# Optimization experiments

Hardware: AMD Instinct MI355X
Metric: run time of the kernel (lower is better)

Reference implementation:

```python
import jax, jax.numpy as jnp
import numpy as np

D_MODEL = 1024
N_HEAD = 16
D_H = D_MODEL // N_HEAD


def setup_inputs() -> dict:
    key = jax.random.key(0)
    ks = jax.random.split(key, 5)
    scale = 1.0 / np.sqrt(D_MODEL)
    x = jax.random.normal(ks[0], (4, 2048, D_MODEL), dtype=jnp.float32)
    # torch nn.Linear weights: shape (out_features, in_features)
    W_qkv = jax.random.uniform(ks[1], (3 * D_MODEL, D_MODEL), dtype=jnp.float32, minval=-scale, maxval=scale)
    b_qkv = jax.random.uniform(ks[2], (3 * D_MODEL,), dtype=jnp.float32, minval=-scale, maxval=scale)
    W_o = jax.random.uniform(ks[3], (D_MODEL, D_MODEL), dtype=jnp.float32, minval=-scale, maxval=scale)
    b_o = jax.random.uniform(ks[4], (D_MODEL,), dtype=jnp.float32, minval=-scale, maxval=scale)
    return {"x": x, "W_qkv": W_qkv, "b_qkv": b_qkv, "W_o": W_o, "b_o": b_o}


def reference(x, W_qkv, b_qkv, W_o, b_o):
    B, S, D = x.shape
    qkv = jnp.einsum('bsd,ed->bse', x, W_qkv) + b_qkv  # [B,S,3D]
    q, k, v = jnp.split(qkv, 3, axis=-1)
    # [B,H,S,d_h]
    q = q.reshape(B, S, N_HEAD, D_H).transpose(0, 2, 1, 3)
    k = k.reshape(B, S, N_HEAD, D_H).transpose(0, 2, 1, 3)
    v = v.reshape(B, S, N_HEAD, D_H).transpose(0, 2, 1, 3)
    sim = jnp.einsum('bhqd,bhkd->bhqk', q, k) / jnp.sqrt(jnp.float32(D_H))
    neg_inf = jnp.finfo(sim.dtype).min
    causal = jnp.tril(jnp.ones((S, S), dtype=bool))
    sim = jnp.where(causal[None, None], sim, neg_inf)
    attn = jax.nn.softmax(sim, axis=-1)
    out = jnp.einsum('bhqk,bhkd->bhqd', attn, v)  # [B,H,S,d_h]
    out = out.transpose(0, 2, 1, 3).reshape(B, S, D)
    return jnp.einsum('bsd,ed->bse', out, W_o) + b_o
```

## Files before the change

kernel.cpp:

```cpp
#include <hip/hip_runtime.h>

#define D_MODEL 1024
#define S_LEN   2048
#define BATCH   4
#define NH      16
#define DH      64
#define M_ROWS  (BATCH * S_LEN)

typedef __attribute__((ext_vector_type(8))) short short8;
typedef __attribute__((ext_vector_type(4))) float floatx4;
typedef unsigned short ushort_t;
typedef __attribute__((ext_vector_type(4))) ushort_t ushortx4;

__device__ __forceinline__ ushort_t f2bf(float f) {
    union { float f; unsigned u; } v; v.f = f;
    unsigned r = v.u + 0x7FFFu + ((v.u >> 16) & 1u);
    return (ushort_t)(r >> 16);
}

__device__ __forceinline__ int pack2(float lo, float hi) {
    return (int)__builtin_amdgcn_perm(__float_as_uint(hi), __float_as_uint(lo), 0x07060302u);
}

__device__ __forceinline__ void async_copy16(const ushort_t* g, ushort_t* l) {
    __builtin_amdgcn_global_load_lds(
        (const __attribute__((address_space(1))) void*)g,
        (__attribute__((address_space(3))) void*)l,
        16, 0, 0);
}

#define N0 (M_ROWS * D_MODEL)
#define N1 (3 * D_MODEL * D_MODEL)
#define N2 (D_MODEL * D_MODEL)
#define NQUADS ((N0 + N1 + N2) / 4)

__global__ __launch_bounds__(256)
void cvt_f32_bf16(const float* __restrict__ s0, const float* __restrict__ s1,
                  const float* __restrict__ s2, ushort_t* __restrict__ d0,
                  ushort_t* __restrict__ d1, ushort_t* __restrict__ d2)
{
    const int q = blockIdx.x * 256 + threadIdx.x;
    if (q >= NQUADS) return;
    const float* s; ushort_t* d; int e;
    if (q < N0 / 4)            { s = s0; d = d0; e = q * 4; }
    else if (q < (N0 + N1) / 4){ s = s1; d = d1; e = q * 4 - N0; }
    else                       { s = s2; d = d2; e = q * 4 - N0 - N1; }
    const float4 v = *(const float4*)&s[e];
    ushortx4 o;
    o[0] = f2bf(v.x); o[1] = f2bf(v.y); o[2] = f2bf(v.z); o[3] = f2bf(v.w);
    *(ushortx4*)&d[e] = o;
}

template<bool F32OUT, bool VSPLIT>
__global__ __launch_bounds__(256)
void gemm_bt_bias(const ushort_t* __restrict__ A, const ushort_t* __restrict__ B,
                  const float* __restrict__ bias, void* __restrict__ Cv,
                  ushort_t* __restrict__ vt, int M, int N, int K)
{
    constexpr int BK = 64;
    constexpr float C2 = 0.18033688011112042f;
    __shared__ ushort_t As[128][BK];
    __shared__ ushort_t Bs[128][BK];

    const int tid  = threadIdx.x;
    const int lane = tid & 63;
    const int wave = tid >> 6;
    const int quad = lane >> 4;
    const int l16  = lane & 15;
    const int bm   = blockIdx.y * 128;
    const int bn   = blockIdx.x * 128;
    const int wm   = (wave & 1) * 64;
    const int wn   = (wave >> 1) * 64;

    floatx4 acc[4][4] = {};

    const int l8r = lane >> 3;
    const int c8  = lane & 7;
    const int swz = l16 & 7;

    for (int k0 = 0; k0 < K; k0 += BK) {
        __syncthreads();
        #pragma unroll
        for (int i = wave; i < 16; i += 4) {
            const int row = i * 8 + l8r;
            const int cc  = (c8 ^ l8r) * 8;
            async_copy16(&A[(size_t)(bm + row) * K + k0 + cc], &As[i * 8][0]);
            async_copy16(&B[(size_t)(bn + row) * K + k0 + cc], &Bs[i * 8][0]);
        }
        __syncthreads();

        #pragma unroll
        for (int h = 0; h < 2; h++) {
            short8 af[4], bfr[4];
            #pragma unroll
            for (int i = 0; i < 4; i++)
                af[i]  = *(const short8*)&As[wm + i * 16 + l16][((h * 4 + quad) ^ swz) * 8];
            #pragma unroll
            for (int i = 0; i < 4; i++)
                bfr[i] = *(const short8*)&Bs[wn + i * 16 + l16][((h * 4 + quad) ^ swz) * 8];

            #pragma unroll
            for (int mi = 0; mi < 4; mi++)
                #pragma unroll
                for (int ni = 0; ni < 4; ni++)
                    acc[mi][ni] = __builtin_amdgcn_mfma_f32_16x16x32_bf16(af[mi], bfr[ni], acc[mi][ni], 0, 0, 0);
        }
    }

    #pragma unroll
    for (int ni = 0; ni < 4; ni++) {
        const int col = bn + wn + ni * 16 + l16;
        const float bv = bias[col];
        #pragma unroll
        for (int mi = 0; mi < 4; mi++)
            #pragma unroll
            for (int r = 0; r < 4; r++) {
                const int row = bm + wm + mi * 16 + quad * 4 + r;
                const float val = acc[mi][ni][r] + bv;
                if (VSPLIT) {
                    if (col < 2 * D_MODEL) {
                        const float vv = (col < D_MODEL) ? val * C2 : val;
                        ((ushort_t*)Cv)[(size_t)row * 2048 + col] = f2bf(vv);
                    } else {
                        const int vcol = col - 2 * D_MODEL;
                        const int h = vcol >> 6, dh = vcol & 63;
                        const int b = row >> 11, s = row & 2047;
                        const int sp = (s & ~63) | ((s & 15) << 2) | ((s >> 4) & 3);
                        vt[(((size_t)(b * NH + h)) * DH + dh) * S_LEN + sp] = f2bf(val);
                    }
                } else if (F32OUT) {
                    ((float*)Cv)[(size_t)row * N + col] = val;
                } else {
                    ((ushort_t*)Cv)[(size_t)row * N + col] = f2bf(val);
                }
            }
    }
}

#define BKV 64

struct TileState {
    short8  qf[2];
    floatx4 o[4];
    float   l[4];
};

__device__ __forceinline__ void attn_tile(
    const ushort_t (*__restrict__ Ks)[DH], const ushort_t (*__restrict__ Vs)[BKV],
    ushort_t* __restrict__ Psw, TileState& st, bool diag,
    int wave, int quad, int l16, int swz, short8 ones)
{
    floatx4 sc[4];
    #pragma unroll
    for (int ns = 0; ns < 4; ns++) {
        const short8 kf0 = *(const short8*)&Ks[ns * 16 + l16][(quad ^ swz) * 8];
        const short8 kf1 = *(const short8*)&Ks[ns * 16 + l16][((4 + quad) ^ swz) * 8];
        floatx4 z = {};
        z = __builtin_amdgcn_mfma_f32_16x16x32_bf16(st.qf[0], kf0, z, 0, 0, 0);
        z = __builtin_amdgcn_mfma_f32_16x16x32_bf16(st.qf[1], kf1, z, 0, 0, 0);
        sc[ns] = z;
    }

    #pragma unroll
    for (int r = 0; r < 4; r++) {
        const int qloc = wave * 16 + quad * 4 + r;
        float p[4];
        #pragma unroll
        for (int ns = 0; ns < 4; ns++) {
            float v = sc[ns][r];
            if (diag) {
                const int kj = ns * 16 + l16;
                v = (kj <= qloc) ? v : -1e30f;
            }
            p[ns] = __builtin_amdgcn_exp2f(v);
        }
        int2 w;
        w.x = pack2(p[0], p[1]);
        w.y = pack2(p[2], p[3]);
        const int row = quad * 4 + r;
        *(int2*)((char*)Psw + row * 128 + (((l16 >> 1) ^ (row & 7)) << 4) + ((l16 & 1) << 3)) = w;
    }

    short8 pf[2];
    #pragma unroll
    for (int c = 0; c < 2; c++)
        pf[c] = *(const short8*)((const char*)Psw + l16 * 128 + ((((c << 2) | quad) ^ (l16 & 7)) << 4));

    floatx4 racc = {};
    racc = __builtin_amdgcn_mfma_f32_16x16x32_bf16(pf[0], ones, racc, 0, 0, 0);
    racc = __builtin_amdgcn_mfma_f32_16x16x32_bf16(pf[1], ones, racc, 0, 0, 0);

    #pragma unroll
    for (int r = 0; r < 4; r++)
        st.l[r] += racc[r];

    #pragma unroll
    for (int d = 0; d < 4; d++) {
        #pragma unroll
        for (int c = 0; c < 2; c++) {
            const short8 vf = *(const short8*)&Vs[d * 16 + l16][((c * 4 + quad) ^ swz) * 8];
            st.o[d] = __builtin_amdgcn_mfma_f32_16x16x32_bf16(pf[c], vf, st.o[d], 0, 0, 0);
        }
    }
}

__device__ __forceinline__ void stage_tile(
    const ushort_t* __restrict__ kg, const ushort_t* __restrict__ vg, int kb,
    ushort_t (*__restrict__ Ksb)[DH], ushort_t (*__restrict__ Vsb)[BKV],
    int wave, int l8r, int c8)
{
    #pragma unroll
    for (int i = wave; i < 8; i += 4) {
        const int row = i * 8 + l8r;
        const int cc  = (c8 ^ l8r) * 8;
        async_copy16(&kg[(size_t)(kb + row) * 2048 + cc], &Ksb[i * 8][0]);
        async_copy16(&vg[(size_t)row * S_LEN + kb + cc], &Vsb[i * 8][0]);
    }
}

__global__ __launch_bounds__(256, 4)
void attn_causal(const ushort_t* __restrict__ qk, const ushort_t* __restrict__ vt,
                 ushort_t* __restrict__ out)
{
    __shared__ ushort_t Ks[2][BKV][DH];
    __shared__ ushort_t Vs[2][DH][BKV];
    __shared__ ushort_t Ps[4][16][64];

    const int tid  = threadIdx.x;
    const int lane = tid & 63;
    const int wave = tid >> 6;
    const int quad = lane >> 4;
    const int l16  = lane & 15;
    const int l8r  = lane >> 3;
    const int c8   = lane & 7;
    const int swz  = l16 & 7;

    const int qa = blockIdx.x;
    const int qb = 31 - qa;
    const int bh = blockIdx.y;
    const int b  = bh >> 4;
    const int h  = bh & 15;

    const size_t qkbase = (size_t)b * S_LEN * 2048;
    const ushort_t* kg = qk + qkbase + D_MODEL + h * DH;
    const ushort_t* vg = vt + (size_t)(b * NH + h) * DH * S_LEN;

    TileState sa, sb;
    #pragma unroll
    for (int r = 0; r < 4; r++) { sa.l[r] = 0.f; sb.l[r] = 0.f; }
    #pragma unroll
    for (int d = 0; d < 4; d++) { sa.o[d] = (floatx4){}; sb.o[d] = (floatx4){}; }

    {
        const ushort_t* qpa = qk + qkbase + (size_t)(qa * 64 + wave * 16 + l16) * 2048 + h * DH;
        sa.qf[0] = *(const short8*)(qpa + quad * 8);
        sa.qf[1] = *(const short8*)(qpa + 32 + quad * 8);
        const ushort_t* qpb = qk + qkbase + (size_t)(qb * 64 + wave * 16 + l16) * 2048 + h * DH;
        sb.qf[0] = *(const short8*)(qpb + quad * 8);
        sb.qf[1] = *(const short8*)(qpb + 32 + quad * 8);
    }

    short8 ones;
    #pragma unroll
    for (int j = 0; j < 8; j++) ones[j] = (short)0x3F80;

    stage_tile(kg, vg, 0, Ks[0], Vs[0], wave, l8r, c8);

    int cur = 0;
    for (int t = 0; t <= qb; t++) {
        __syncthreads();
        if (t < qb)
            stage_tile(kg, vg, (t + 1) * BKV, Ks[cur ^ 1], Vs[cur ^ 1], wave, l8r, c8);

        if (t <= qa) attn_tile(Ks[cur], Vs[cur], &Ps[wave][0][0], sa, t == qa, wave, quad, l16, swz, ones);
        attn_tile(Ks[cur], Vs[cur], &Ps[wave][0][0], sb, t == qb, wave, quad, l16, swz, ones);
        cur ^= 1;
    }

    #pragma unroll
    for (int r = 0; r < 4; r++) {
        const float inva = 1.0f / sa.l[r];
        const float invb = 1.0f / sb.l[r];
        const int ra = qa * 64 + wave * 16 + quad * 4 + r;
        const int rb = qb * 64 + wave * 16 + quad * 4 + r;
        #pragma unroll
        for (int d = 0; d < 4; d++) {
            out[(size_t)(b * S_LEN + ra) * D_MODEL + h * DH + d * 16 + l16] = f2bf(sa.o[d][r] * inva);
            out[(size_t)(b * S_LEN + rb) * D_MODEL + h * DH + d * 16 + l16] = f2bf(sb.o[d][r] * invb);
        }
    }
}

extern "C" void kernel_launch(void* const* d_in, const int* in_sizes, int n_in,
                              void* d_out, int out_size, void* d_ws, size_t ws_size,
                              hipStream_t stream)
{
    const float* x    = (const float*)d_in[0];
    const float* Wqkv = (const float*)d_in[1];
    const float* bqkv = (const float*)d_in[2];
    const float* Wo   = (const float*)d_in[3];
    const float* bo   = (const float*)d_in[4];
    float* out = (float*)d_out;

    ushort_t* xb    = (ushort_t*)d_ws;
    ushort_t* wqkvb = xb + N0;
    ushort_t* wob   = wqkvb + N1;
    ushort_t* qkbuf = wob + N2;
    ushort_t* vtbuf = qkbuf + (size_t)M_ROWS * 2048;
    ushort_t* att   = vtbuf + (size_t)BATCH * NH * DH * S_LEN;

    dim3 blk(256);
    cvt_f32_bf16<<<dim3((NQUADS + 255) / 256), blk, 0, stream>>>(x, Wqkv, Wo, xb, wqkvb, wob);
    gemm_bt_bias<false, true><<<dim3((3 * D_MODEL) / 128, M_ROWS / 128), blk, 0, stream>>>(
        xb, wqkvb, bqkv, qkbuf, vtbuf, M_ROWS, 3 * D_MODEL, D_MODEL);
    attn_causal<<<dim3(16, BATCH * NH), blk, 0, stream>>>(qkbuf, vtbuf, att);
    gemm_bt_bias<true, false><<<dim3(D_MODEL / 128, M_ROWS / 128), blk, 0, stream>>>(
        att, wob, bo, out, nullptr, M_ROWS, D_MODEL, D_MODEL);
}
```

Before: 264.1 us.

## Use 8-wave GEMM blocks, XCD-aware block remapping, and MFMA priority hints in attention

The GEMM moves from 256 to 512 threads per block. Each wave now computes a 64x32 sub-tile, which halves its accumulators and spreads tile loading across more waves. Both the GEMMs and the attention kernel remap block IDs so that neighbouring tiles or heads land on the same XCD, aiming for better L2 reuse. The attention kernel also wraps its MFMA sections in s_setprio to favour the matrix work. Costs are more LDS read traffic per FLOP in the GEMM and extra index arithmetic.

```diff
diff --git a/kernel.cpp b/kernel.cpp
--- a/kernel.cpp
+++ b/kernel.cpp
@@ -52,10 +52,10 @@
 }
 
 template<bool F32OUT, bool VSPLIT>
-__global__ __launch_bounds__(256)
-void gemm_bt_bias(const ushort_t* __restrict__ A, const ushort_t* __restrict__ B,
-                  const float* __restrict__ bias, void* __restrict__ Cv,
-                  ushort_t* __restrict__ vt, int M, int N, int K)
+__global__ __launch_bounds__(512, 4)
+void gemm_bt(const ushort_t* __restrict__ A, const ushort_t* __restrict__ B,
+             const float* __restrict__ bias, void* __restrict__ Cv,
+             ushort_t* __restrict__ vt, int M, int N, int K)
 {
     constexpr int BK = 64;
     constexpr float C2 = 0.18033688011112042f;
@@ -67,21 +67,26 @@
     const int wave = tid >> 6;
     const int quad = lane >> 4;
     const int l16  = lane & 15;
-    const int bm   = blockIdx.y * 128;
-    const int bn   = blockIdx.x * 128;
-    const int wm   = (wave & 1) * 64;
-    const int wn   = (wave >> 1) * 64;
-
-    floatx4 acc[4][4] = {};
-
-    const int l8r = lane >> 3;
-    const int c8  = lane & 7;
-    const int swz = l16 & 7;
+    const int l8r  = lane >> 3;
+    const int c8   = lane & 7;
+    const int swz  = l16 & 7;
+
+    const int gdx = gridDim.x;
+    const int bid = blockIdx.y * gdx + blockIdx.x;
+    const int nwg = gdx * gridDim.y;
+    const int sw  = (bid & 7) * (nwg >> 3) + (bid >> 3);
+    const int bm  = (sw / gdx) * 128;
+    const int bn  = (sw % gdx) * 128;
+
+    const int wm = (wave & 1) * 64;
+    const int wn = (wave >> 1) * 32;
+
+    floatx4 acc[4][2] = {};
 
     for (int k0 = 0; k0 < K; k0 += BK) {
         __syncthreads();
         #pragma unroll
-        for (int i = wave; i < 16; i += 4) {
+        for (int i = wave; i < 16; i += 8) {
             const int row = i * 8 + l8r;
             const int cc  = (c8 ^ l8r) * 8;
             async_copy16(&A[(size_t)(bm + row) * K + k0 + cc], &As[i * 8][0]);
@@ -91,24 +96,24 @@
 
         #pragma unroll
         for (int h = 0; h < 2; h++) {
-            short8 af[4], bfr[4];
+            short8 af[4], bfr[2];
             #pragma unroll
             for (int i = 0; i < 4; i++)
                 af[i]  = *(const short8*)&As[wm + i * 16 + l16][((h * 4 + quad) ^ swz) * 8];
             #pragma unroll
-            for (int i = 0; i < 4; i++)
+            for (int i = 0; i < 2; i++)
                 bfr[i] = *(const short8*)&Bs[wn + i * 16 + l16][((h * 4 + quad) ^ swz) * 8];
 
             #pragma unroll
             for (int mi = 0; mi < 4; mi++)
                 #pragma unroll
-                for (int ni = 0; ni < 4; ni++)
+                for (int ni = 0; ni < 2; ni++)
                     acc[mi][ni] = __builtin_amdgcn_mfma_f32_16x16x32_bf16(af[mi], bfr[ni], acc[mi][ni], 0, 0, 0);
         }
     }
 
     #pragma unroll
-    for (int ni = 0; ni < 4; ni++) {
+    for (int ni = 0; ni < 2; ni++) {
         const int col = bn + wn + ni * 16 + l16;
         const float bv = bias[col];
         #pragma unroll
@@ -124,8 +129,8 @@
                     } else {
                         const int vcol = col - 2 * D_MODEL;
                         const int h = vcol >> 6, dh = vcol & 63;
-                        const int b = row >> 11, s = row & 2047;
-                        const int sp = (s & ~63) | ((s & 15) << 2) | ((s >> 4) & 3);
+                        const int b = row >> 11, s2 = row & 2047;
+                        const int sp = (s2 & ~63) | ((s2 & 15) << 2) | ((s2 >> 4) & 3);
                         vt[(((size_t)(b * NH + h)) * DH + dh) * S_LEN + sp] = f2bf(val);
                     }
                 } else if (F32OUT) {
@@ -151,6 +156,7 @@
     int wave, int quad, int l16, int swz, short8 ones)
 {
     floatx4 sc[4];
+    __builtin_amdgcn_s_setprio(1);
     #pragma unroll
     for (int ns = 0; ns < 4; ns++) {
         const short8 kf0 = *(const short8*)&Ks[ns * 16 + l16][(quad ^ swz) * 8];
@@ -160,6 +166,7 @@
         z = __builtin_amdgcn_mfma_f32_16x16x32_bf16(st.qf[1], kf1, z, 0, 0, 0);
         sc[ns] = z;
     }
+    __builtin_amdgcn_s_setprio(0);
 
     #pragma unroll
     for (int r = 0; r < 4; r++) {
@@ -186,6 +193,7 @@
     for (int c = 0; c < 2; c++)
         pf[c] = *(const short8*)((const char*)Psw + l16 * 128 + ((((c << 2) | quad) ^ (l16 & 7)) << 4));
 
+    __builtin_amdgcn_s_setprio(1);
     floatx4 racc = {};
     racc = __builtin_amdgcn_mfma_f32_16x16x32_bf16(pf[0], ones, racc, 0, 0, 0);
     racc = __builtin_amdgcn_mfma_f32_16x16x32_bf16(pf[1], ones, racc, 0, 0, 0);
@@ -202,6 +210,7 @@
             st.o[d] = __builtin_amdgcn_mfma_f32_16x16x32_bf16(pf[c], vf, st.o[d], 0, 0, 0);
         }
     }
+    __builtin_amdgcn_s_setprio(0);
 }
 
 __device__ __forceinline__ void stage_tile(
@@ -235,11 +244,13 @@
     const int c8   = lane & 7;
     const int swz  = l16 & 7;
 
-    const int qa = blockIdx.x;
-    const int qb = 31 - qa;
-    const int bh = blockIdx.y;
-    const int b  = bh >> 4;
-    const int h  = bh & 15;
+    const int id  = blockIdx.y * 16 + blockIdx.x;
+    const int sid = (id & 7) * 128 + (id >> 3);
+    const int qa  = sid & 15;
+    const int qb  = 31 - qa;
+    const int bh  = sid >> 4;
+    const int b   = bh >> 4;
+    const int h   = bh & 15;
 
     const size_t qkbase = (size_t)b * S_LEN * 2048;
     const ushort_t* kg = qk + qkbase + D_MODEL + h * DH;
@@ -309,11 +320,12 @@
     ushort_t* vtbuf = qkbuf + (size_t)M_ROWS * 2048;
     ushort_t* att   = vtbuf + (size_t)BATCH * NH * DH * S_LEN;
 
-    dim3 blk(256);
-    cvt_f32_bf16<<<dim3((NQUADS + 255) / 256), blk, 0, stream>>>(x, Wqkv, Wo, xb, wqkvb, wob);
-    gemm_bt_bias<false, true><<<dim3((3 * D_MODEL) / 128, M_ROWS / 128), blk, 0, stream>>>(
+    cvt_f32_bf16<<<dim3((NQUADS + 255) / 256), dim3(256), 0, stream>>>(x, Wqkv, Wo, xb, wqkvb, wob);
+    gemm_bt<false, true>
+        <<<dim3((3 * D_MODEL) / 128, M_ROWS / 128), dim3(512), 0, stream>>>(
         xb, wqkvb, bqkv, qkbuf, vtbuf, M_ROWS, 3 * D_MODEL, D_MODEL);
-    attn_causal<<<dim3(16, BATCH * NH), blk, 0, stream>>>(qkbuf, vtbuf, att);
-    gemm_bt_bias<true, false><<<dim3(D_MODEL / 128, M_ROWS / 128), blk, 0, stream>>>(
+    attn_causal<<<dim3(16, BATCH * NH), dim3(256), 0, stream>>>(qkbuf, vtbuf, att);
+    gemm_bt<true, false>
+        <<<dim3(D_MODEL / 128, M_ROWS / 128), dim3(512), 0, stream>>>(
         att, wob, bo, out, nullptr, M_ROWS, D_MODEL, D_MODEL);
 }
```

New measurement: 257.8 us. 2.4% less time.
